# Optimization experiments

Hardware: AMD Instinct MI355X
Metric: run time of the kernel (lower is better)

## Reference

```python
import jax, jax.numpy as jnp
import numpy as np

NUM_HEADS = 32
NUM_KV_HEADS = 8
HEAD_DIM = 128
PAGE_SIZE = 16
NUM_PAGES = 512
PAGES_PER_SEQ = 256  # 4096 cached tokens
Q_LEN = 1024
SCALE = 0.08838834764831845  # 1/sqrt(HEAD_DIM)


def setup_inputs() -> dict:
    key = jax.random.key(0)
    k1, k2, k3, k4, k5 = jax.random.split(key, 5)
    q = jax.random.normal(k1, (Q_LEN, NUM_HEADS * HEAD_DIM), dtype=jnp.float32)
    k = jax.random.normal(k2, (Q_LEN, NUM_KV_HEADS * HEAD_DIM), dtype=jnp.float32)
    v = jax.random.normal(k3, (Q_LEN, NUM_KV_HEADS * HEAD_DIM), dtype=jnp.float32)
    # paged KV cache: [num_pages, 2 (k/v), num_kv_heads, page_size, head_dim]
    kv_cache = jax.random.normal(
        k4, (NUM_PAGES, 2, NUM_KV_HEADS, PAGE_SIZE, HEAD_DIM), dtype=jnp.float32)
    block_table = jnp.sort(
        jax.random.randint(k5, (PAGES_PER_SEQ,), 0, NUM_PAGES, dtype=jnp.int32))
    return {"q": q, "k": k, "v": v, "kv_cache": kv_cache,
            "block_table": block_table}


def reference(q, k, v, kv_cache, block_table):
    # reshape flat projections into heads
    q = q.reshape(-1, NUM_HEADS, HEAD_DIM)          # [Tq, H, D]
    k = k.reshape(-1, NUM_KV_HEADS, HEAD_DIM)       # [Tq, Hkv, D]
    v = v.reshape(-1, NUM_KV_HEADS, HEAD_DIM)

    # gather paged KV cache into continuous tensors (all pages full)
    pages = kv_cache[block_table]                   # [P, 2, Hkv, ps, D]
    # per-page [Hkv, ps, D] -> [ps, Hkv, D], then concat along token dim
    past = jnp.transpose(pages, (1, 0, 3, 2, 4))    # [2, P, ps, Hkv, D]
    past = past.reshape(2, -1, NUM_KV_HEADS, HEAD_DIM)
    past_k, past_v = past[0], past[1]               # [Tpast, Hkv, D]

    k_full = jnp.concatenate([past_k, k], axis=0)   # [Tkv, Hkv, D]
    v_full = jnp.concatenate([past_v, v], axis=0)

    # GQA: repeat kv heads to match query heads
    heads_per_kv = NUM_HEADS // NUM_KV_HEADS
    k_full = jnp.repeat(k_full, heads_per_kv, axis=1)  # [Tkv, H, D]
    v_full = jnp.repeat(v_full, heads_per_kv, axis=1)

    qh = jnp.transpose(q, (1, 0, 2))                # [H, Tq, D]
    kh = jnp.transpose(k_full, (1, 0, 2))           # [H, Tkv, D]
    vh = jnp.transpose(v_full, (1, 0, 2))

    scores = jnp.einsum('hqd,hkd->hqk', qh, kh) * SCALE  # [H, Tq, Tkv]

    # prefill causal mask exactly as in the source: triu(ones(q_len, kv_len), 1)
    q_len, kv_len = qh.shape[1], kh.shape[1]
    causal = jnp.triu(jnp.ones((q_len, kv_len), dtype=bool), k=1)
    scores = jnp.where(causal[None, :, :], -jnp.inf, scores)

    attn = jax.nn.softmax(scores.astype(jnp.float32), axis=-1).astype(qh.dtype)
    out = jnp.einsum('hqk,hkd->hqd', attn, vh)      # [H, Tq, D]
    out = jnp.transpose(out, (1, 0, 2)).reshape(-1, NUM_HEADS * HEAD_DIM)
    return out
```

## Files before the change

kernel.cpp:

```cpp
#include <hip/hip_runtime.h>
#include <hip/hip_bf16.h>


#define NUM_HEADS 32
#define HEAD_DIM 128
#define Q_STRIDE 4096
#define SCALE 0.08838834764831845f
#define RESCALE_THR 8.0f
#define KSW_TILE 16384
#define VSW_OFF (2 * 1024 * 1024)

typedef short short8 __attribute__((ext_vector_type(8)));
typedef float f32x4 __attribute__((ext_vector_type(4)));
typedef unsigned short ushort_t;
typedef unsigned int uint_t;

__device__ __forceinline__ ushort_t f2bf(float f) {
    return __builtin_bit_cast(ushort_t, __float2bfloat16(f));
}
__device__ __forceinline__ uint_t pk2(float a, float b) {
    return (uint_t)f2bf(a) | ((uint_t)f2bf(b) << 16);
}

__launch_bounds__(256)
__global__ void prep_kv(const float* __restrict__ kvc,
                        const int* __restrict__ bt,
                        char* __restrict__ wsb)
{
    __shared__ float sVt[64 * 128];
    const int blk = blockIdx.x;
    const int hkv = blk >> 4;
    const int jb  = blk & 15;
    const int tid = threadIdx.x;
    char* kout = wsb + (size_t)(hkv * 16 + jb) * KSW_TILE;
    char* vout = wsb + VSW_OFF + (size_t)(hkv * 16 + jb) * KSW_TILE;

#pragma unroll
    for (int i = 0; i < 4; ++i) {
        const int u = tid + i * 256;
        const int t = u >> 4, c = u & 15;
        const int gtok = jb * 64 + t;
        const int page = bt[gtok >> 4];
        const float* src = kvc + (size_t)page * 32768 + (size_t)hkv * 2048
                         + (gtok & 15) * 128 + c * 8;
        float4 a = *(const float4*)src;
        float4 b = *(const float4*)(src + 4);
        uint4 p;
        p.x = pk2(a.x, a.y); p.y = pk2(a.z, a.w);
        p.z = pk2(b.x, b.y); p.w = pk2(b.z, b.w);
        *(uint4*)(kout + t * 256 + ((c * 16) ^ ((t & 7) << 4))) = p;
    }
#pragma unroll
    for (int i = 0; i < 8; ++i) {
        const int u = tid + i * 256;
        const int t = u >> 5, c4 = u & 31;
        const int gtok = jb * 64 + t;
        const int page = bt[gtok >> 4];
        const float* src = kvc + (size_t)page * 32768 + 16384
                         + (size_t)hkv * 2048 + (gtok & 15) * 128 + c4 * 4;
        *(float4*)(sVt + t * 128 + c4 * 4) = *(const float4*)src;
    }
    __syncthreads();
#pragma unroll
    for (int i = 0; i < 4; ++i) {
        const int u = tid + i * 256;
        const int d = u >> 3, ch = u & 7;
        float v[8];
#pragma unroll
        for (int k = 0; k < 8; ++k) v[k] = sVt[(8 * ch + k) * 128 + d];
        uint4 p;
        p.x = pk2(v[0], v[1]); p.y = pk2(v[2], v[3]);
        p.z = pk2(v[4], v[5]); p.w = pk2(v[6], v[7]);
        *(uint4*)(vout + ((d * 128 + 16 * ch) ^ ((d & 7) << 4))) = p;
    }
}

#define GLL16(G, L) __builtin_amdgcn_global_load_lds(                         \
    (const uint_t __attribute__((address_space(1)))*)(G),                     \
    (uint_t __attribute__((address_space(3)))*)(L), 16, 0, 0)

#define STAGE(JB, KB, VB) {                                                   \
    const char* ks = kvbf + (size_t)(hkv * 16 + (JB)) * KSW_TILE              \
                   + w * 4096 + lane * 16;                                    \
    const char* vs = ks + VSW_OFF;                                            \
    _Pragma("unroll")                                                         \
    for (int i = 0; i < 4; ++i) {                                             \
        GLL16(ks + i * 1024, (KB) + w * 4096 + i * 1024);                     \
        GLL16(vs + i * 1024, (VB) + w * 4096 + i * 1024);                     \
    }                                                                         \
}

__launch_bounds__(256)
__global__ void attn_main(const float* __restrict__ q,
                          const char* __restrict__ kvbf,
                          float* __restrict__ out)
{
    __shared__ __align__(16) char sK[2][16384];
    __shared__ __align__(16) char sV[2][16384];
    __shared__ __align__(16) char sP[4][2048];

    const int bid = blockIdx.x;
    const int h   = bid & 31;
    const int qt  = 15 - (bid >> 5);
    const int hkv = h >> 2;
    const int tid  = threadIdx.x;
    const int w    = tid >> 6;
    const int lane = tid & 63;
    const int l15  = lane & 15;
    const int lhi  = lane >> 4;

    short8 qf[4];
    {
        const int qrow = qt * 64 + w * 16 + l15;
        const float* qp = q + (size_t)qrow * Q_STRIDE + h * HEAD_DIM;
#pragma unroll
        for (int s = 0; s < 4; ++s) {
            const int d0 = s * 32 + lhi * 8;
            float4 a = *(const float4*)(qp + d0);
            float4 b = *(const float4*)(qp + d0 + 4);
            short8 v;
            v[0] = (short)f2bf(a.x * SCALE); v[1] = (short)f2bf(a.y * SCALE);
            v[2] = (short)f2bf(a.z * SCALE); v[3] = (short)f2bf(a.w * SCALE);
            v[4] = (short)f2bf(b.x * SCALE); v[5] = (short)f2bf(b.y * SCALE);
            v[6] = (short)f2bf(b.z * SCALE); v[7] = (short)f2bf(b.w * SCALE);
            qf[s] = v;
        }
    }

    f32x4 acc[8];
#pragma unroll
    for (int n2 = 0; n2 < 8; ++n2) acc[n2] = (f32x4){0.f, 0.f, 0.f, 0.f};
    float m_run[4]  = {-1e30f, -1e30f, -1e30f, -1e30f};
    float l_part[4] = {0.f, 0.f, 0.f, 0.f};

    STAGE(0, sK[0], sV[0])
    __syncthreads();

    for (int jb = 0; jb <= qt; ++jb) {
        const int cur = jb & 1;
        char* kbuf = sK[cur];
        char* vbuf = sV[cur];
        const bool pf = (jb < qt);
        if (pf) {
            STAGE(jb + 1, sK[cur ^ 1], sV[cur ^ 1])
        }

        f32x4 sacc[4];
#pragma unroll
        for (int n = 0; n < 4; ++n) sacc[n] = (f32x4){0.f, 0.f, 0.f, 0.f};
#pragma unroll
        for (int s = 0; s < 4; ++s) {
#pragma unroll
            for (int n = 0; n < 4; ++n) {
                const int tok = n * 16 + l15;
                const uint_t byte = (uint_t)(tok * 256)
                    + (((uint_t)((s * 32 + lhi * 8) * 2)) ^ ((uint_t)((tok & 7) << 4)));
                short8 kb = *(const short8*)(kbuf + byte);
                sacc[n] = __builtin_amdgcn_mfma_f32_16x16x32_bf16(qf[s], kb, sacc[n], 0, 0, 0);
            }
        }

        const bool diag = (jb == qt);
        float pv[4][4];
#pragma unroll
        for (int n = 0; n < 4; ++n)
#pragma unroll
            for (int j = 0; j < 4; ++j) {
                float x = sacc[n][j];
                if (diag) {
                    const int tok = jb * 64 + n * 16 + l15;
                    const int qg  = qt * 64 + w * 16 + lhi * 4 + j;
                    if (tok > qg) x = -1e30f;
                }
                pv[n][j] = x;
            }
#pragma unroll
        for (int j = 0; j < 4; ++j) {
            float lmax = fmaxf(fmaxf(pv[0][j], pv[1][j]), fmaxf(pv[2][j], pv[3][j]));
            if (__any(lmax > m_run[j] + RESCALE_THR)) {
                float mt = lmax;
#pragma unroll
                for (int off = 1; off < 16; off <<= 1)
                    mt = fmaxf(mt, __shfl_xor(mt, off));
                const float mn = fmaxf(m_run[j], mt);
                const float alpha = __expf(m_run[j] - mn);
                m_run[j] = mn;
                l_part[j] *= alpha;
#pragma unroll
                for (int n2 = 0; n2 < 8; ++n2) acc[n2][j] *= alpha;
            }
            float ls = 0.f;
#pragma unroll
            for (int n = 0; n < 4; ++n) {
                float p = __expf(pv[n][j] - m_run[j]);
                pv[n][j] = p;
                ls += p;
            }
            l_part[j] += ls;
        }

        char* pb = sP[w];
#pragma unroll
        for (int n = 0; n < 4; ++n)
#pragma unroll
            for (int j = 0; j < 4; ++j) {
                const int r = lhi * 4 + j;
                const uint_t byte = (uint_t)(r * 128)
                    + (((uint_t)((n * 16 + l15) * 2)) ^ ((uint_t)((r & 7) << 4)));
                *(ushort_t*)(pb + byte) = f2bf(pv[n][j]);
            }

#pragma unroll
        for (int s2 = 0; s2 < 2; ++s2) {
            const uint_t pbyte = (uint_t)(l15 * 128)
                + (((uint_t)((s2 * 32 + lhi * 8) * 2)) ^ ((uint_t)((l15 & 7) << 4)));
            short8 pa = *(const short8*)(pb + pbyte);
#pragma unroll
            for (int n2 = 0; n2 < 8; ++n2) {
                const int dim = n2 * 16 + l15;
                const uint_t vbyte = (uint_t)(dim * 128)
                    + (((uint_t)((s2 * 32 + lhi * 8) * 2)) ^ ((uint_t)((dim & 7) << 4)));
                short8 vbf = *(const short8*)(vbuf + vbyte);
                acc[n2] = __builtin_amdgcn_mfma_f32_16x16x32_bf16(pa, vbf, acc[n2], 0, 0, 0);
            }
        }

        if (pf) __syncthreads();
    }

#pragma unroll
    for (int j = 0; j < 4; ++j) {
        float lsum = l_part[j];
#pragma unroll
        for (int off = 1; off < 16; off <<= 1)
            lsum += __shfl_xor(lsum, off);
        const float inv = 1.0f / lsum;
        const int qg = qt * 64 + w * 16 + lhi * 4 + j;
        float* dst = out + (size_t)qg * Q_STRIDE + h * HEAD_DIM;
#pragma unroll
        for (int n2 = 0; n2 < 8; ++n2)
            dst[n2 * 16 + l15] = acc[n2][j] * inv;
    }
}

extern "C" void kernel_launch(void* const* d_in, const int* in_sizes, int n_in,
                              void* d_out, int out_size, void* d_ws, size_t ws_size,
                              hipStream_t stream) {
    const float* q   = (const float*)d_in[0];
    const float* kvc = (const float*)d_in[3];
    const int*   bt  = (const int*)d_in[4];
    float* out = (float*)d_out;
    char*  wsb = (char*)d_ws;
    prep_kv<<<dim3(128), dim3(256), 0, stream>>>(kvc, bt, wsb);
    attn_main<<<dim3(512), dim3(256), 0, stream>>>(q, wsb, out);
}
```

Before: 45.80 us.

## Prefetch KV through registers into single LDS buffer, use exp2 softmax and setprio

Replaces the double-buffered direct global-to-LDS async loads with register prefetch of the next K/V tile, written into a single shared buffer between two barriers at the end of each iteration. This halves LDS use, which may allow more resident blocks. The log2(e) factor is folded into the Q scale so the softmax can use exp2f. s_setprio is raised around the MFMA loops. The trade-off is extra register pressure and an additional barrier plus LDS store pass on every iteration.

```diff
diff --git a/kernel.cpp b/kernel.cpp
--- a/kernel.cpp
+++ b/kernel.cpp
@@ -2,10 +2,8 @@
 #include <hip/hip_bf16.h>
 
 
-#define NUM_HEADS 32
-#define HEAD_DIM 128
 #define Q_STRIDE 4096
-#define SCALE 0.08838834764831845f
+#define SCALE2 0.1275179114285314f
 #define RESCALE_THR 8.0f
 #define KSW_TILE 16384
 #define VSW_OFF (2 * 1024 * 1024)
@@ -79,24 +77,13 @@
     (const uint_t __attribute__((address_space(1)))*)(G),                     \
     (uint_t __attribute__((address_space(3)))*)(L), 16, 0, 0)
 
-#define STAGE(JB, KB, VB) {                                                   \
-    const char* ks = kvbf + (size_t)(hkv * 16 + (JB)) * KSW_TILE              \
-                   + w * 4096 + lane * 16;                                    \
-    const char* vs = ks + VSW_OFF;                                            \
-    _Pragma("unroll")                                                         \
-    for (int i = 0; i < 4; ++i) {                                             \
-        GLL16(ks + i * 1024, (KB) + w * 4096 + i * 1024);                     \
-        GLL16(vs + i * 1024, (VB) + w * 4096 + i * 1024);                     \
-    }                                                                         \
-}
-
 __launch_bounds__(256)
 __global__ void attn_main(const float* __restrict__ q,
                           const char* __restrict__ kvbf,
                           float* __restrict__ out)
 {
-    __shared__ __align__(16) char sK[2][16384];
-    __shared__ __align__(16) char sV[2][16384];
+    __shared__ __align__(16) char sK[16384];
+    __shared__ __align__(16) char sV[16384];
     __shared__ __align__(16) char sP[4][2048];
 
     const int bid = blockIdx.x;
@@ -112,17 +99,17 @@
     short8 qf[4];
     {
         const int qrow = qt * 64 + w * 16 + l15;
-        const float* qp = q + (size_t)qrow * Q_STRIDE + h * HEAD_DIM;
+        const float* qp = q + (size_t)qrow * Q_STRIDE + h * 128;
 #pragma unroll
         for (int s = 0; s < 4; ++s) {
             const int d0 = s * 32 + lhi * 8;
             float4 a = *(const float4*)(qp + d0);
             float4 b = *(const float4*)(qp + d0 + 4);
             short8 v;
-            v[0] = (short)f2bf(a.x * SCALE); v[1] = (short)f2bf(a.y * SCALE);
-            v[2] = (short)f2bf(a.z * SCALE); v[3] = (short)f2bf(a.w * SCALE);
-            v[4] = (short)f2bf(b.x * SCALE); v[5] = (short)f2bf(b.y * SCALE);
-            v[6] = (short)f2bf(b.z * SCALE); v[7] = (short)f2bf(b.w * SCALE);
+            v[0] = (short)f2bf(a.x * SCALE2); v[1] = (short)f2bf(a.y * SCALE2);
+            v[2] = (short)f2bf(a.z * SCALE2); v[3] = (short)f2bf(a.w * SCALE2);
+            v[4] = (short)f2bf(b.x * SCALE2); v[5] = (short)f2bf(b.y * SCALE2);
+            v[6] = (short)f2bf(b.z * SCALE2); v[7] = (short)f2bf(b.w * SCALE2);
             qf[s] = v;
         }
     }
@@ -133,21 +120,39 @@
     float m_run[4]  = {-1e30f, -1e30f, -1e30f, -1e30f};
     float l_part[4] = {0.f, 0.f, 0.f, 0.f};
 
-    STAGE(0, sK[0], sV[0])
+    {
+        const char* b0 = kvbf + (size_t)(hkv * 16) * KSW_TILE + w * 4096 + lane * 16;
+#pragma unroll
+        for (int i = 0; i < 4; ++i) {
+            GLL16(b0 + i * 1024,           sK + w * 4096 + i * 1024);
+            GLL16(b0 + VSW_OFF + i * 1024, sV + w * 4096 + i * 1024);
+        }
+    }
     __syncthreads();
 
+    char* pb = sP[w];
     for (int jb = 0; jb <= qt; ++jb) {
-        const int cur = jb & 1;
-        char* kbuf = sK[cur];
-        char* vbuf = sV[cur];
         const bool pf = (jb < qt);
+
+        float4 kr0, kr1, kr2, kr3, vr0, vr1, vr2, vr3;
         if (pf) {
-            STAGE(jb + 1, sK[cur ^ 1], sV[cur ^ 1])
+            const char* nb = kvbf + (size_t)(hkv * 16 + jb + 1) * KSW_TILE
+                           + w * 4096 + lane * 16;
+            kr0 = *(const float4*)(nb);
+            kr1 = *(const float4*)(nb + 1024);
+            kr2 = *(const float4*)(nb + 2048);
+            kr3 = *(const float4*)(nb + 3072);
+            const char* nv = nb + VSW_OFF;
+            vr0 = *(const float4*)(nv);
+            vr1 = *(const float4*)(nv + 1024);
+            vr2 = *(const float4*)(nv + 2048);
+            vr3 = *(const float4*)(nv + 3072);
         }
 
         f32x4 sacc[4];
 #pragma unroll
         for (int n = 0; n < 4; ++n) sacc[n] = (f32x4){0.f, 0.f, 0.f, 0.f};
+        __builtin_amdgcn_s_setprio(1);
 #pragma unroll
         for (int s = 0; s < 4; ++s) {
 #pragma unroll
@@ -155,35 +160,34 @@
                 const int tok = n * 16 + l15;
                 const uint_t byte = (uint_t)(tok * 256)
                     + (((uint_t)((s * 32 + lhi * 8) * 2)) ^ ((uint_t)((tok & 7) << 4)));
-                short8 kb = *(const short8*)(kbuf + byte);
+                short8 kb = *(const short8*)(sK + byte);
                 sacc[n] = __builtin_amdgcn_mfma_f32_16x16x32_bf16(qf[s], kb, sacc[n], 0, 0, 0);
             }
         }
+        __builtin_amdgcn_s_setprio(0);
 
         const bool diag = (jb == qt);
-        float pv[4][4];
-#pragma unroll
-        for (int n = 0; n < 4; ++n)
-#pragma unroll
-            for (int j = 0; j < 4; ++j) {
-                float x = sacc[n][j];
-                if (diag) {
+        if (diag) {
+#pragma unroll
+            for (int n = 0; n < 4; ++n)
+#pragma unroll
+                for (int j = 0; j < 4; ++j) {
                     const int tok = jb * 64 + n * 16 + l15;
                     const int qg  = qt * 64 + w * 16 + lhi * 4 + j;
-                    if (tok > qg) x = -1e30f;
+                    if (tok > qg) sacc[n][j] = -1e30f;
                 }
-                pv[n][j] = x;
-            }
+        }
 #pragma unroll
         for (int j = 0; j < 4; ++j) {
-            float lmax = fmaxf(fmaxf(pv[0][j], pv[1][j]), fmaxf(pv[2][j], pv[3][j]));
+            float lmax = fmaxf(fmaxf(sacc[0][j], sacc[1][j]),
+                               fmaxf(sacc[2][j], sacc[3][j]));
             if (__any(lmax > m_run[j] + RESCALE_THR)) {
                 float mt = lmax;
 #pragma unroll
                 for (int off = 1; off < 16; off <<= 1)
                     mt = fmaxf(mt, __shfl_xor(mt, off));
                 const float mn = fmaxf(m_run[j], mt);
-                const float alpha = __expf(m_run[j] - mn);
+                const float alpha = exp2f(m_run[j] - mn);
                 m_run[j] = mn;
                 l_part[j] *= alpha;
 #pragma unroll
@@ -192,14 +196,13 @@
             float ls = 0.f;
 #pragma unroll
             for (int n = 0; n < 4; ++n) {
-                float p = __expf(pv[n][j] - m_run[j]);
-                pv[n][j] = p;
+                float p = exp2f(sacc[n][j] - m_run[j]);
+                sacc[n][j] = p;
                 ls += p;
             }
             l_part[j] += ls;
         }
 
-        char* pb = sP[w];
 #pragma unroll
         for (int n = 0; n < 4; ++n)
 #pragma unroll
@@ -207,9 +210,10 @@
                 const int r = lhi * 4 + j;
                 const uint_t byte = (uint_t)(r * 128)
                     + (((uint_t)((n * 16 + l15) * 2)) ^ ((uint_t)((r & 7) << 4)));
-                *(ushort_t*)(pb + byte) = f2bf(pv[n][j]);
-            }
-
+                *(ushort_t*)(pb + byte) = f2bf(sacc[n][j]);
+            }
+
+        __builtin_amdgcn_s_setprio(1);
 #pragma unroll
         for (int s2 = 0; s2 < 2; ++s2) {
             const uint_t pbyte = (uint_t)(l15 * 128)
@@ -220,12 +224,24 @@
                 const int dim = n2 * 16 + l15;
                 const uint_t vbyte = (uint_t)(dim * 128)
                     + (((uint_t)((s2 * 32 + lhi * 8) * 2)) ^ ((uint_t)((dim & 7) << 4)));
-                short8 vbf = *(const short8*)(vbuf + vbyte);
+                short8 vbf = *(const short8*)(sV + vbyte);
                 acc[n2] = __builtin_amdgcn_mfma_f32_16x16x32_bf16(pa, vbf, acc[n2], 0, 0, 0);
             }
         }
-
-        if (pf) __syncthreads();
+        __builtin_amdgcn_s_setprio(0);
+
+        if (pf) {
+            __syncthreads();
+            *(float4*)(sK + w * 4096 + lane * 16)        = kr0;
+            *(float4*)(sK + w * 4096 + 1024 + lane * 16) = kr1;
+            *(float4*)(sK + w * 4096 + 2048 + lane * 16) = kr2;
+            *(float4*)(sK + w * 4096 + 3072 + lane * 16) = kr3;
+            *(float4*)(sV + w * 4096 + lane * 16)        = vr0;
+            *(float4*)(sV + w * 4096 + 1024 + lane * 16) = vr1;
+            *(float4*)(sV + w * 4096 + 2048 + lane * 16) = vr2;
+            *(float4*)(sV + w * 4096 + 3072 + lane * 16) = vr3;
+            __syncthreads();
+        }
     }
 
 #pragma unroll
@@ -236,7 +252,7 @@
             lsum += __shfl_xor(lsum, off);
         const float inv = 1.0f / lsum;
         const int qg = qt * 64 + w * 16 + lhi * 4 + j;
-        float* dst = out + (size_t)qg * Q_STRIDE + h * HEAD_DIM;
+        float* dst = out + (size_t)qg * Q_STRIDE + h * 128;
 #pragma unroll
         for (int n2 = 0; n2 < 8; ++n2)
             dst[n2 * 16 + l15] = acc[n2][j] * inv;
```

Result: no change. 46.28 us (+1.1%).
